# Optimization experiments

Hardware: AMD Instinct MI355X
Metric: run time of the kernel (lower is better)

The kernel has to match this reference:

```python
import jax, jax.numpy as jnp
import numpy as np

B, H, WD, C = 16, 96, 96, 256
WS, SH, NH = 6, 3, 8
N = WS * WS
ALPHA = (2 * 6) ** 0.25  # deepnorm alpha, n_layers=6
SCALE = (C // NH) ** 0.5  # faithful to source: head_dim**0.5 (not **-0.5)
EPS = 1e-5


def _rel_index(ws):
    coords = np.stack(np.meshgrid(np.arange(ws), np.arange(ws), indexing='ij'))  # (2,ws,ws)
    flat = coords.reshape(2, -1)
    rel = (flat[:, :, None] - flat[:, None, :]).transpose(1, 2, 0).copy()
    rel[..., 0] += ws - 1
    rel[..., 1] += ws - 1
    rel[..., 0] *= 2 * ws - 1
    return jnp.asarray(rel.sum(-1))  # (N,N) int


def _attn_mask(h, w, ws, sh):
    img = np.zeros((h, w))
    cnt = 0
    for hs in (slice(0, -ws), slice(-ws, -sh), slice(-sh, None)):
        for wsl in (slice(0, -ws), slice(-ws, -sh), slice(-sh, None)):
            img[hs, wsl] = cnt
            cnt += 1
    win = img.reshape(h // ws, ws, w // ws, ws).transpose(0, 2, 1, 3).reshape(-1, ws * ws)
    diff = win[:, None, :] - win[:, :, None]
    return jnp.asarray(np.where(diff != 0, -100.0, 0.0), jnp.float32)  # (nW,N,N)


def _ln(t, w, b):
    mu = jnp.mean(t, -1, keepdims=True)
    var = jnp.var(t, -1, keepdims=True)
    return (t - mu) * jax.lax.rsqrt(var + EPS) * w + b


def setup_inputs() -> dict:
    key = jax.random.key(0)
    ks = jax.random.split(key, 8)
    d = {
        'x': jax.random.normal(ks[0], (B, H * WD, C), jnp.float32),
        'qkv_w': jax.random.normal(ks[1], (C, 3 * C), jnp.float32) * 0.02,
        'qkv_b': jnp.zeros((3 * C,), jnp.float32),
        'bias_table': jax.random.normal(ks[2], ((2 * WS - 1) ** 2, NH), jnp.float32) * 0.02,
        'proj_w': jax.random.normal(ks[3], (C, C), jnp.float32) * 0.02,
        'proj_b': jnp.zeros((C,), jnp.float32),
        'norm1_w': jnp.ones((C,), jnp.float32),
        'norm1_b': jnp.zeros((C,), jnp.float32),
        'norm2_w': jnp.ones((C,), jnp.float32),
        'norm2_b': jnp.zeros((C,), jnp.float32),
        'fc1_w': jax.random.normal(ks[4], (C, 4 * C), jnp.float32) * 0.02,
        'fc1_b': jnp.zeros((4 * C,), jnp.float32),
        'fc2_w': jax.random.normal(ks[5], (4 * C, C), jnp.float32) * 0.02,
        'fc2_b': jnp.zeros((C,), jnp.float32),
    }
    return d


def reference(x, qkv_w, qkv_b, bias_table, proj_w, proj_b, norm1_w, norm1_b,
              norm2_w, norm2_b, fc1_w, fc1_b, fc2_w, fc2_b):
    hd = C // NH
    nW = (H // WS) * (WD // WS)
    shortcut = x  # (B, L, C), norm_before=False -> post-norm
    xs = x.reshape(B, H, WD, C)
    xs = jnp.roll(xs, (-SH, -SH), axis=(1, 2))  # cyclic shift
    # window partition -> (B*nW, N, C)
    xw = xs.reshape(B, H // WS, WS, WD // WS, WS, C).transpose(0, 1, 3, 2, 4, 5).reshape(B * nW, N, C)
    qkv = (xw @ qkv_w + qkv_b).reshape(B * nW, N, 3, NH, hd).transpose(2, 0, 3, 1, 4)
    q, k, v = qkv[0] * SCALE, qkv[1], qkv[2]
    attn = jnp.einsum('bhnd,bhmd->bhnm', q, k)  # (B*nW, H, N, N)
    bias = bias_table[_rel_index(WS).reshape(-1)].reshape(N, N, NH).transpose(2, 0, 1)
    attn = attn + bias[None]
    mask = _attn_mask(H, WD, WS, SH)  # (nW, N, N)
    attn = attn.reshape(B, nW, NH, N, N) + mask[None, :, None]
    attn = jax.nn.softmax(attn.reshape(B * nW, NH, N, N), axis=-1)
    out = jnp.einsum('bhnm,bhmd->bhnd', attn, v).transpose(0, 2, 1, 3).reshape(B * nW, N, C)
    out = out @ proj_w + proj_b
    # faithful buggy window_reverse: identity permute == plain reshape
    xs = out.reshape(B, H // WS, WS, WD // WS, WS, C).reshape(B, H, WD, C)
    xs = jnp.roll(xs, (SH, SH), axis=(1, 2))
    x1 = _ln(shortcut * ALPHA + xs.reshape(B, H * WD, C), norm1_w, norm1_b)
    hmid = jax.nn.gelu(x1 @ fc1_w + fc1_b, approximate=False)
    x2 = _ln(x1 * ALPHA + (hmid @ fc2_w + fc2_b), norm2_w, norm2_b)
    return x2
```

## Files before the change

kernel.cpp:

```cpp
#include <hip/hip_runtime.h>
#include <math.h>

typedef __bf16 bf16x8 __attribute__((ext_vector_type(8)));
typedef __bf16 bf16x4 __attribute__((ext_vector_type(4)));
typedef short  s16x4  __attribute__((ext_vector_type(4)));
typedef float  f32x4  __attribute__((ext_vector_type(4)));

#define NTOK 147456
#define LTOK 9216
#define ALPHA 1.8612097182041991f
#define QSCALE 5.656854249492380196f
#define MFMA32(a,b,c) __builtin_amdgcn_mfma_f32_16x16x32_bf16((a),(b),(c),0,0,0)
#define SWB(row,kb) ((kb) ^ ((row)&7))

__device__ __forceinline__ f32x4 MFMA16(bf16x4 a, bf16x4 b, f32x4 c) {
#if __has_builtin(__builtin_amdgcn_mfma_f32_16x16x16bf16_1k)
    return __builtin_amdgcn_mfma_f32_16x16x16bf16_1k(*(s16x4*)&a, *(s16x4*)&b, c, 0, 0, 0);
#else
    f32x4 d = c;
    asm volatile("s_nop 1\n\ts_nop 1\n\t"
                 "v_mfma_f32_16x16x16_bf16 %0, %1, %2, %0\n\t"
                 "s_nop 7\n\ts_nop 7"
                 : "+v"(d) : "v"(a), "v"(b));
    return d;
#endif
}

__device__ __forceinline__ float gelu_sig(float x) {
    const float e = __expf(-1.702f * x);
    return x * __builtin_amdgcn_rcpf(1.0f + e);
}

__device__ __forceinline__ void gll16(const void* g, void* l) {
    __builtin_amdgcn_global_load_lds(
        (const __attribute__((address_space(1))) void*)g,
        (__attribute__((address_space(3))) void*)l, 16, 0, 0);
}

__global__ __launch_bounds__(256) void k0_prep(
    const float* __restrict__ qkv_w, const float* __restrict__ proj_w,
    const float* __restrict__ fc1_w, const float* __restrict__ fc2_w,
    __bf16* __restrict__ qkvT, __bf16* __restrict__ projT,
    __bf16* __restrict__ w1T, __bf16* __restrict__ w2T)
{
    const int id = blockIdx.x * 256 + threadIdx.x;
    if (id < 196608) {
        const int o = id >> 8, k = id & 255;
        qkvT[id] = (__bf16)qkv_w[k * 768 + o];
    } else if (id < 262144) {
        const int i = id - 196608, o = i >> 8, k = i & 255;
        projT[i] = (__bf16)proj_w[k * 256 + o];
    } else if (id < 524288) {
        const int i = id - 262144, o = i >> 8, k = i & 255;
        w1T[i] = (__bf16)fc1_w[k * 1024 + o];
    } else {
        const int i = id - 524288, o = i >> 10, k = i & 1023;
        w2T[i] = (__bf16)fc2_w[k * 256 + o];
    }
}

__global__ __launch_bounds__(512, 4) void k1f_qkv_attn(
    const float* __restrict__ x, const __bf16* __restrict__ qkvT,
    const float* __restrict__ qkv_b, const float* __restrict__ bias_table,
    __bf16* __restrict__ attnout)
{
    __shared__ __attribute__((aligned(16))) char SM[77824];
    typedef __bf16 (*a256_t)[256];
    typedef __bf16 (*b32_t)[32];
    a256_t As = (a256_t)SM;
    b32_t  Bs = (b32_t)(SM + 24576);
    int*   srcrow = (int*)(SM + 73728);
    float* bias_s = (float*)(SM + 73920);

    const int t = threadIdx.x;
    const int wid = t >> 6, lane = t & 63;
    const int l15 = lane & 15, lg = lane >> 4;
    const int blk = blockIdx.x;
    const int win = blk & 255;
    const int wh = win >> 4, ww = win & 15;
    const int h = wid;

    if (t < 48) {
        int n = t; if (n > 35) n = 35;
        const int b = blk >> 8;
        const int gh = (wh * 6 + n / 6 + 3) % 96;
        const int gw = (ww * 6 + n % 6 + 3) % 96;
        srcrow[t] = b * LTOK + gh * 96 + gw;
    }
    for (int o = t; o < 968; o += 512) bias_s[o] = bias_table[o];
    __syncthreads();

    for (int o = t; o < 48 * 32; o += 512) {
        const int row = o >> 5, kb = o & 31;
        const float* src = x + (size_t)srcrow[row] * 256 + kb * 8;
        const float4 f0 = *(const float4*)src;
        const float4 f1 = *(const float4*)(src + 4);
        bf16x8 p;
        p[0] = (__bf16)f0.x; p[1] = (__bf16)f0.y; p[2] = (__bf16)f0.z; p[3] = (__bf16)f0.w;
        p[4] = (__bf16)f1.x; p[5] = (__bf16)f1.y; p[6] = (__bf16)f1.z; p[7] = (__bf16)f1.w;
        *(bf16x8*)&As[row][SWB(row, kb) * 8] = p;
    }

    const f32x4 fzero = {0.f, 0.f, 0.f, 0.f};
    f32x4 accQ[2][3], accK[2][3], accV[2][3];
    #pragma unroll
    for (int c = 0; c < 2; ++c)
        #pragma unroll
        for (int r = 0; r < 3; ++r) { accQ[c][r] = fzero; accK[c][r] = fzero; accV[c][r] = fzero; }

    for (int kc = 0; kc < 8; ++kc) {
        __syncthreads();
        #pragma unroll
        for (int i = 0; i < 6; ++i) {
            const int r0 = wid * 96 + i * 16;
            const int row = r0 + (lane >> 2), kbl = lane & 3;
            gll16(qkvT + (size_t)row * 256 + kc * 32 + ((kbl ^ (row & 3)) * 8),
                  &Bs[r0][0]);
        }
        __syncthreads();
        bf16x8 af[3];
        #pragma unroll
        for (int rt = 0; rt < 3; ++rt) {
            const int ar = rt * 16 + l15;
            const int kb = kc * 4 + lg;
            af[rt] = *(const bf16x8*)&As[ar][SWB(ar, kb) * 8];
        }
        #pragma unroll
        for (int ct = 0; ct < 2; ++ct) {
            const int brq = h * 32 + ct * 16 + l15;
            const bf16x8 bq = *(const bf16x8*)&Bs[brq][((lg ^ (brq & 3))) * 8];
            const int brk = 256 + brq;
            const bf16x8 bk = *(const bf16x8*)&Bs[brk][((lg ^ (brk & 3))) * 8];
            const int brv = 512 + brq;
            const bf16x8 bv = *(const bf16x8*)&Bs[brv][((lg ^ (brv & 3))) * 8];
            #pragma unroll
            for (int rt = 0; rt < 3; ++rt) {
                accQ[ct][rt] = MFMA32(bq, af[rt], accQ[ct][rt]);
                accK[ct][rt] = MFMA32(bk, af[rt], accK[ct][rt]);
                accV[ct][rt] = MFMA32(af[rt], bv, accV[ct][rt]);
            }
        }
    }

    bf16x4 qf[3][2], kf[3][2], vf[2][3];
    #pragma unroll
    for (int dh = 0; dh < 2; ++dh) {
        #pragma unroll
        for (int q = 0; q < 4; ++q) {
            const float qb = qkv_b[h * 32 + dh * 16 + lg * 4 + q];
            const float kb = qkv_b[256 + h * 32 + dh * 16 + lg * 4 + q];
            #pragma unroll
            for (int rt = 0; rt < 3; ++rt) {
                qf[rt][dh][q] = (__bf16)((accQ[dh][rt][q] + qb) * QSCALE);
                kf[rt][dh][q] = (__bf16)(accK[dh][rt][q] + kb);
            }
        }
    }
    #pragma unroll
    for (int cd = 0; cd < 2; ++cd) {
        const float vb = qkv_b[512 + h * 32 + cd * 16 + l15];
        #pragma unroll
        for (int c3 = 0; c3 < 3; ++c3)
            #pragma unroll
            for (int q = 0; q < 4; ++q)
                vf[cd][c3][q] = (__bf16)(accV[cd][c3][q] + vb);
    }

    f32x4 s[3][3];
    #pragma unroll
    for (int qt = 0; qt < 3; ++qt)
        #pragma unroll
        for (int c3 = 0; c3 < 3; ++c3) {
            f32x4 acc = MFMA16(kf[c3][0], qf[qt][0], fzero);
            s[qt][c3] = MFMA16(kf[c3][1], qf[qt][1], acc);
        }

    int i2_[3][4], j2_[3][4], g2_[3][4];
    #pragma unroll
    for (int c3 = 0; c3 < 3; ++c3)
        #pragma unroll
        for (int q = 0; q < 4; ++q) {
            const int kt = c3 * 16 + lg * 4 + q;
            const int kk2 = kt < 36 ? kt : 35;
            i2_[c3][q] = kk2 / 6; j2_[c3][q] = kk2 - i2_[c3][q] * 6;
            g2_[c3][q] = ((wh < 15) ? 0 : (i2_[c3][q] < 3 ? 1 : 2)) * 3
                       + ((ww < 15) ? 0 : (j2_[c3][q] < 3 ? 1 : 2));
        }

    bf16x4 pa[3][3];
    #pragma unroll
    for (int qt = 0; qt < 3; ++qt) {
        const int qtok = qt * 16 + l15;
        const int nn = qtok < 36 ? qtok : 35;
        const int i1 = nn / 6, j1 = nn - i1 * 6;
        const int g1 = ((wh < 15) ? 0 : (i1 < 3 ? 1 : 2)) * 3
                     + ((ww < 15) ? 0 : (j1 < 3 ? 1 : 2));
        float vals[3][4];
        float mx = -1e30f;
        #pragma unroll
        for (int c3 = 0; c3 < 3; ++c3)
            #pragma unroll
            for (int q = 0; q < 4; ++q) {
                const int kt = c3 * 16 + lg * 4 + q;
                float v;
                if (kt < 36) {
                    v = s[qt][c3][q]
                      + bias_s[((i1 - i2_[c3][q] + 5) * 11 + (j1 - j2_[c3][q] + 5)) * 8 + h];
                    if (g1 != g2_[c3][q]) v -= 100.0f;
                } else {
                    v = -1e30f;
                }
                vals[c3][q] = v;
                mx = fmaxf(mx, v);
            }
        mx = fmaxf(mx, __shfl_xor(mx, 16));
        mx = fmaxf(mx, __shfl_xor(mx, 32));
        float sum = 0.f;
        #pragma unroll
        for (int c3 = 0; c3 < 3; ++c3)
            #pragma unroll
            for (int q = 0; q < 4; ++q) {
                const float e = __expf(vals[c3][q] - mx);
                vals[c3][q] = e;
                sum += e;
            }
        sum += __shfl_xor(sum, 16);
        sum += __shfl_xor(sum, 32);
        const float inv = 1.0f / sum;
        #pragma unroll
        for (int c3 = 0; c3 < 3; ++c3)
            #pragma unroll
            for (int q = 0; q < 4; ++q)
                pa[qt][c3][q] = (__bf16)(vals[c3][q] * inv);
    }

    const size_t rowbase = (size_t)blk * 36;
    #pragma unroll
    for (int qt = 0; qt < 3; ++qt)
        #pragma unroll
        for (int cd = 0; cd < 2; ++cd) {
            f32x4 o = MFMA16(pa[qt][0], vf[cd][0], fzero);
            o = MFMA16(pa[qt][1], vf[cd][1], o);
            o = MFMA16(pa[qt][2], vf[cd][2], o);
            #pragma unroll
            for (int q = 0; q < 4; ++q) {
                const int n = qt * 16 + lg * 4 + q;
                if (n < 36)
                    attnout[(rowbase + n) * 256 + h * 32 + cd * 16 + l15] = (__bf16)o[q];
            }
        }
}

__global__ __launch_bounds__(512) void k2_proj_ln(
    const __bf16* __restrict__ attnout, const __bf16* __restrict__ projT,
    const float* __restrict__ proj_b, const float* __restrict__ x,
    const float* __restrict__ n1w, const float* __restrict__ n1b,
    __bf16* __restrict__ x1b)
{
    __shared__ __attribute__((aligned(16))) __bf16 As[128][64];
    __shared__ __attribute__((aligned(16))) __bf16 Bs[256][64];
    __shared__ float ps[128][4], ps2[128][4];
    const int t = threadIdx.x;
    const int wid = t >> 6, lane = t & 63;
    const int l15 = lane & 15, lg = lane >> 4;
    const int mb = blockIdx.x;
    const int wm = wid >> 2, wn = wid & 3;

    const f32x4 fzero = {0.f, 0.f, 0.f, 0.f};
    f32x4 acc[4][4];
    #pragma unroll
    for (int i = 0; i < 4; ++i)
        #pragma unroll
        for (int j = 0; j < 4; ++j) acc[i][j] = fzero;

    for (int kc = 0; kc < 4; ++kc) {
        __syncthreads();
        #pragma unroll
        for (int i = 0; i < 2; ++i) {
            const int r0 = wid * 16 + i * 8;
            const int row = r0 + (lane >> 3), kbl = lane & 7;
            gll16(attnout + (size_t)(mb * 128 + row) * 256 + kc * 64 + ((kbl ^ (row & 7)) * 8),
                  &As[r0][0]);
        }
        #pragma unroll
        for (int i = 0; i < 4; ++i) {
            const int r0 = wid * 32 + i * 8;
            const int row = r0 + (lane >> 3), kbl = lane & 7;
            gll16(projT + (size_t)row * 256 + kc * 64 + ((kbl ^ (row & 7)) * 8),
                  &Bs[r0][0]);
        }
        __syncthreads();
        #pragma unroll
        for (int kk = 0; kk < 2; ++kk) {
            bf16x8 af[4], bfr[4];
            #pragma unroll
            for (int rt = 0; rt < 4; ++rt) {
                const int ar = wm * 64 + rt * 16 + l15;
                af[rt] = *(const bf16x8*)&As[ar][((kk * 4 + lg) ^ (ar & 7)) * 8];
            }
            #pragma unroll
            for (int ct = 0; ct < 4; ++ct) {
                const int br = wn * 64 + ct * 16 + l15;
                bfr[ct] = *(const bf16x8*)&Bs[br][((kk * 4 + lg) ^ (br & 7)) * 8];
            }
            #pragma unroll
            for (int rt = 0; rt < 4; ++rt)
                #pragma unroll
                for (int ct = 0; ct < 4; ++ct)
                    acc[rt][ct] = MFMA32(af[rt], bfr[ct], acc[rt][ct]);
        }
    }

    int dtok_[4][4];
    #pragma unroll
    for (int rt = 0; rt < 4; ++rt) {
        #pragma unroll
        for (int q = 0; q < 4; ++q) {
            const int rowl = wm * 64 + rt * 16 + lg * 4 + q;
            const int tok = mb * 128 + rowl;
            const int b = tok / LTOK, l = tok % LTOK;
            const int hh = l / 96, wwp = l % 96;
            const int dtok = b * LTOK + ((hh + 3) % 96) * 96 + ((wwp + 3) % 96);
            dtok_[rt][q] = dtok;
            float s = 0.f, s2 = 0.f;
            #pragma unroll
            for (int ct = 0; ct < 4; ++ct) {
                const int col = wn * 64 + ct * 16 + l15;
                const float v = acc[rt][ct][q] + proj_b[col] + ALPHA * x[(size_t)dtok * 256 + col];
                acc[rt][ct][q] = v;
                s += v; s2 += v * v;
            }
            s  += __shfl_xor(s, 1, 16);  s += __shfl_xor(s, 2, 16);
            s  += __shfl_xor(s, 4, 16);  s += __shfl_xor(s, 8, 16);
            s2 += __shfl_xor(s2, 1, 16); s2 += __shfl_xor(s2, 2, 16);
            s2 += __shfl_xor(s2, 4, 16); s2 += __shfl_xor(s2, 8, 16);
            if (l15 == 0) { ps[rowl][wn] = s; ps2[rowl][wn] = s2; }
        }
    }
    __syncthreads();
    #pragma unroll
    for (int rt = 0; rt < 4; ++rt) {
        #pragma unroll
        for (int q = 0; q < 4; ++q) {
            const int rowl = wm * 64 + rt * 16 + lg * 4 + q;
            const float S  = ps[rowl][0] + ps[rowl][1] + ps[rowl][2] + ps[rowl][3];
            const float S2 = ps2[rowl][0] + ps2[rowl][1] + ps2[rowl][2] + ps2[rowl][3];
            const float mu = S * (1.0f / 256.0f);
            const float var = S2 * (1.0f / 256.0f) - mu * mu;
            const float rstd = rsqrtf(var + 1e-5f);
            __bf16* op = x1b + (size_t)dtok_[rt][q] * 256;
            #pragma unroll
            for (int ct = 0; ct < 4; ++ct) {
                const int col = wn * 64 + ct * 16 + l15;
                op[col] = (__bf16)((acc[rt][ct][q] - mu) * rstd * n1w[col] + n1b[col]);
            }
        }
    }
}

__global__ __launch_bounds__(512, 2) void k3f_mlp(
    const __bf16* __restrict__ x1b, const __bf16* __restrict__ w1T,
    const float* __restrict__ fc1_b, const __bf16* __restrict__ w2T,
    const float* __restrict__ fc2_b, const float* __restrict__ n2w,
    const float* __restrict__ n2b, float* __restrict__ out)
{
    __shared__ __attribute__((aligned(16))) __bf16 w1c[2][64][256];
    __shared__ __attribute__((aligned(16))) __bf16 w2c[2][256][64];
    __shared__ float ps[128][2], ps2[128][2];

    const int t = threadIdx.x;
    const int wid = t >> 6, lane = t & 63;
    const int l15 = lane & 15, lg = lane >> 4;
    const int rg = wid >> 1, chs = wid & 1;
    const int rowbase = blockIdx.x * 128 + rg * 32;

    bf16x8 af[2][8];
    #pragma unroll
    for (int tt = 0; tt < 2; ++tt)
        #pragma unroll
        for (int kk = 0; kk < 8; ++kk)
            af[tt][kk] = *(const bf16x8*)(x1b + (size_t)(rowbase + tt * 16 + l15) * 256 + kk * 32 + lg * 8);

    const f32x4 fzero = {0.f, 0.f, 0.f, 0.f};
    f32x4 acc2[2][8];
    #pragma unroll
    for (int i = 0; i < 2; ++i)
        #pragma unroll
        for (int j = 0; j < 8; ++j) acc2[i][j] = fzero;

    #define STAGE_W(b, c)                                                       \
    {                                                                           \
        _Pragma("unroll")                                                       \
        for (int i = 0; i < 4; ++i) {                                           \
            const int r0 = wid * 8 + i * 2;                                     \
            const int row = r0 + (lane >> 5);                                   \
            const int g = (lane & 31) ^ (row & 7);                              \
            gll16(w1T + (size_t)((c) * 64 + row) * 256 + g * 8, &w1c[b][r0][0]);\
        }                                                                       \
        _Pragma("unroll")                                                       \
        for (int i = 0; i < 4; ++i) {                                           \
            const int r0 = wid * 32 + i * 8;                                    \
            const int row = r0 + (lane >> 3);                                   \
            const int g = (lane & 7) ^ (row & 7);                               \
            gll16(w2T + (size_t)row * 1024 + (c) * 64 + g * 8, &w2c[b][r0][0]); \
        }                                                                       \
    }

    STAGE_W(0, 0);
    __syncthreads();

    for (int ch = 0; ch < 16; ++ch) {
        const int cur = ch & 1;
        if (ch < 15) STAGE_W(cur ^ 1, ch + 1);

        f32x4 acc1[4][2];
        #pragma unroll
        for (int i = 0; i < 4; ++i)
            #pragma unroll
            for (int j = 0; j < 2; ++j) acc1[i][j] = fzero;
        #pragma unroll
        for (int kk = 0; kk < 8; ++kk) {
            #pragma unroll
            for (int ht = 0; ht < 4; ++ht) {
                const int hr = ht * 16 + l15;
                const bf16x8 aW = *(const bf16x8*)&w1c[cur][hr][((kk * 4 + lg) ^ (hr & 7)) * 8];
                #pragma unroll
                for (int tt = 0; tt < 2; ++tt)
                    acc1[ht][tt] = MFMA32(aW, af[tt][kk], acc1[ht][tt]);
            }
        }

        bf16x4 a16[2][4];
        #pragma unroll
        for (int ht = 0; ht < 4; ++ht) {
            float bq[4];
            #pragma unroll
            for (int q = 0; q < 4; ++q)
                bq[q] = fc1_b[ch * 64 + ht * 16 + lg * 4 + q];
            #pragma unroll
            for (int tt = 0; tt < 2; ++tt)
                #pragma unroll
                for (int q = 0; q < 4; ++q)
                    a16[tt][ht][q] = (__bf16)gelu_sig(acc1[ht][tt][q] + bq[q]);
        }

        #pragma unroll
        for (int ht = 0; ht < 4; ++ht) {
            #pragma unroll
            for (int ct = 0; ct < 8; ++ct) {
                const int br = chs * 128 + ct * 16 + l15;
                const bf16x4 bW = *(const bf16x4*)&w2c[cur][br]
                    [((ht * 2 + (lg >> 1)) ^ (br & 7)) * 8 + (lg & 1) * 4];
                #pragma unroll
                for (int tt = 0; tt < 2; ++tt)
                    acc2[tt][ct] = MFMA16(a16[tt][ht], bW, acc2[tt][ct]);
            }
        }

        __syncthreads();
    }

    #pragma unroll
    for (int tt = 0; tt < 2; ++tt) {
        #pragma unroll
        for (int q = 0; q < 4; ++q) {
            const int grow = rg * 32 + tt * 16 + lg * 4 + q;
            const size_t tok = (size_t)(blockIdx.x * 128 + grow);
            float s = 0.f, s2 = 0.f;
            #pragma unroll
            for (int ct = 0; ct < 8; ++ct) {
                const int col = chs * 128 + ct * 16 + l15;
                const float v = acc2[tt][ct][q] + fc2_b[col] + ALPHA * (float)x1b[tok * 256 + col];
                acc2[tt][ct][q] = v;
                s += v; s2 += v * v;
            }
            s  += __shfl_xor(s, 1, 16);  s += __shfl_xor(s, 2, 16);
            s  += __shfl_xor(s, 4, 16);  s += __shfl_xor(s, 8, 16);
            s2 += __shfl_xor(s2, 1, 16); s2 += __shfl_xor(s2, 2, 16);
            s2 += __shfl_xor(s2, 4, 16); s2 += __shfl_xor(s2, 8, 16);
            if (l15 == 0) { ps[grow][chs] = s; ps2[grow][chs] = s2; }
        }
    }
    __syncthreads();
    #pragma unroll
    for (int tt = 0; tt < 2; ++tt) {
        #pragma unroll
        for (int q = 0; q < 4; ++q) {
            const int grow = rg * 32 + tt * 16 + lg * 4 + q;
            const size_t tok = (size_t)(blockIdx.x * 128 + grow);
            const float S  = ps[grow][0] + ps[grow][1];
            const float S2 = ps2[grow][0] + ps2[grow][1];
            const float mu = S * (1.0f / 256.0f);
            const float var = S2 * (1.0f / 256.0f) - mu * mu;
            const float rstd = rsqrtf(var + 1e-5f);
            float* op = out + tok * 256;
            #pragma unroll
            for (int ct = 0; ct < 8; ++ct) {
                const int col = chs * 128 + ct * 16 + l15;
                op[col] = (acc2[tt][ct][q] - mu) * rstd * n2w[col] + n2b[col];
            }
        }
    }
    #undef STAGE_W
}

extern "C" void kernel_launch(void* const* d_in, const int* in_sizes, int n_in,
                              void* d_out, int out_size, void* d_ws, size_t ws_size,
                              hipStream_t stream)
{
    const float* x          = (const float*)d_in[0];
    const float* qkv_w      = (const float*)d_in[1];
    const float* qkv_b      = (const float*)d_in[2];
    const float* bias_table = (const float*)d_in[3];
    const float* proj_w     = (const float*)d_in[4];
    const float* proj_b     = (const float*)d_in[5];
    const float* n1w        = (const float*)d_in[6];
    const float* n1b        = (const float*)d_in[7];
    const float* n2w        = (const float*)d_in[8];
    const float* n2b        = (const float*)d_in[9];
    const float* fc1_w      = (const float*)d_in[10];
    const float* fc1_b      = (const float*)d_in[11];
    const float* fc2_w      = (const float*)d_in[12];
    const float* fc2_b      = (const float*)d_in[13];
    float* out = (float*)d_out;

    char* ws = (char*)d_ws;
    __bf16* x1b     = (__bf16*)ws;
    __bf16* attnout = (__bf16*)(ws + 75497472);
    __bf16* qkvT    = (__bf16*)(ws + 150994944);
    __bf16* projT   = (__bf16*)(ws + 151388160);
    __bf16* w1T     = (__bf16*)(ws + 151519232);
    __bf16* w2T     = (__bf16*)(ws + 152043520);

    k0_prep<<<3072, 256, 0, stream>>>(qkv_w, proj_w, fc1_w, fc2_w, qkvT, projT, w1T, w2T);
    k1f_qkv_attn<<<4096, 512, 0, stream>>>(x, qkvT, qkv_b, bias_table, attnout);
    k2_proj_ln<<<1152, 512, 0, stream>>>(attnout, projT, proj_b, x, n1w, n1b, x1b);
    k3f_mlp<<<1152, 512, 0, stream>>>(x1b, w1T, fc1_b, w2T, fc2_b, n2w, n2b, out);
}
```

Before: 733.8 us.

## Restructure MLP kernel to 4 waves with full-width rows and LDS-staged hidden

```diff
diff --git a/kernel.cpp b/kernel.cpp
--- a/kernel.cpp
+++ b/kernel.cpp
@@ -358,21 +358,20 @@
     }
 }
 
-__global__ __launch_bounds__(512, 2) void k3f_mlp(
+__global__ __launch_bounds__(256, 2) void k3f_mlp(
     const __bf16* __restrict__ x1b, const __bf16* __restrict__ w1T,
     const float* __restrict__ fc1_b, const __bf16* __restrict__ w2T,
     const float* __restrict__ fc2_b, const float* __restrict__ n2w,
     const float* __restrict__ n2b, float* __restrict__ out)
 {
-    __shared__ __attribute__((aligned(16))) __bf16 w1c[2][64][256];
-    __shared__ __attribute__((aligned(16))) __bf16 w2c[2][256][64];
-    __shared__ float ps[128][2], ps2[128][2];
+    __shared__ __attribute__((aligned(16))) __bf16 w1c[2][32][256];
+    __shared__ __attribute__((aligned(16))) __bf16 w2c[2][256][32];
+    __shared__ __attribute__((aligned(16))) __bf16 hs[4][32][32];
 
     const int t = threadIdx.x;
-    const int wid = t >> 6, lane = t & 63;
+    const int wv = t >> 6, lane = t & 63;
     const int l15 = lane & 15, lg = lane >> 4;
-    const int rg = wid >> 1, chs = wid & 1;
-    const int rowbase = blockIdx.x * 128 + rg * 32;
+    const int rowbase = blockIdx.x * 128 + wv * 32;
 
     bf16x8 af[2][8];
     #pragma unroll
@@ -382,46 +381,49 @@
             af[tt][kk] = *(const bf16x8*)(x1b + (size_t)(rowbase + tt * 16 + l15) * 256 + kk * 32 + lg * 8);
 
     const f32x4 fzero = {0.f, 0.f, 0.f, 0.f};
-    f32x4 acc2[2][8];
+    f32x4 acc2[2][16];
     #pragma unroll
     for (int i = 0; i < 2; ++i)
         #pragma unroll
-        for (int j = 0; j < 8; ++j) acc2[i][j] = fzero;
-
-    #define STAGE_W(b, c)                                                       \
-    {                                                                           \
-        _Pragma("unroll")                                                       \
-        for (int i = 0; i < 4; ++i) {                                           \
-            const int r0 = wid * 8 + i * 2;                                     \
-            const int row = r0 + (lane >> 5);                                   \
-            const int g = (lane & 31) ^ (row & 7);                              \
-            gll16(w1T + (size_t)((c) * 64 + row) * 256 + g * 8, &w1c[b][r0][0]);\
-        }                                                                       \
-        _Pragma("unroll")                                                       \
-        for (int i = 0; i < 4; ++i) {                                           \
-            const int r0 = wid * 32 + i * 8;                                    \
-            const int row = r0 + (lane >> 3);                                   \
-            const int g = (lane & 7) ^ (row & 7);                               \
-            gll16(w2T + (size_t)row * 1024 + (c) * 64 + g * 8, &w2c[b][r0][0]); \
-        }                                                                       \
+        for (int j = 0; j < 16; ++j) acc2[i][j] = fzero;
+
+    #define STAGE_W(b, c)                                                        \
+    {                                                                            \
+        _Pragma("unroll")                                                        \
+        for (int i = 0; i < 4; ++i) {                                            \
+            const int r0 = wv * 8 + i * 2;                                       \
+            const int row = r0 + (lane >> 5);                                    \
+            const int g = (lane & 31) ^ (row & 7);                               \
+            gll16(w1T + (size_t)((c) * 32 + row) * 256 + g * 8, &w1c[b][r0][0]); \
+        }                                                                        \
+        _Pragma("unroll")                                                        \
+        for (int i = 0; i < 4; ++i) {                                            \
+            const int r0 = wv * 64 + i * 16;                                     \
+            const int row = r0 + (lane >> 2);                                    \
+            const int g = (lane & 3) ^ (row & 3);                                \
+            gll16(w2T + (size_t)row * 1024 + (c) * 32 + g * 8, &w2c[b][r0][0]);  \
+        }                                                                        \
     }
 
     STAGE_W(0, 0);
-    __syncthreads();
-
-    for (int ch = 0; ch < 16; ++ch) {
+    asm volatile("s_waitcnt vmcnt(0)" ::: "memory");
+    __builtin_amdgcn_sched_barrier(0);
+    __builtin_amdgcn_s_barrier();
+    __builtin_amdgcn_sched_barrier(0);
+
+    for (int ch = 0; ch < 32; ++ch) {
         const int cur = ch & 1;
-        if (ch < 15) STAGE_W(cur ^ 1, ch + 1);
-
-        f32x4 acc1[4][2];
-        #pragma unroll
-        for (int i = 0; i < 4; ++i)
+        if (ch < 31) STAGE_W(cur ^ 1, ch + 1);
+
+        f32x4 acc1[2][2];
+        #pragma unroll
+        for (int i = 0; i < 2; ++i)
             #pragma unroll
             for (int j = 0; j < 2; ++j) acc1[i][j] = fzero;
         #pragma unroll
         for (int kk = 0; kk < 8; ++kk) {
             #pragma unroll
-            for (int ht = 0; ht < 4; ++ht) {
+            for (int ht = 0; ht < 2; ++ht) {
                 const int hr = ht * 16 + l15;
                 const bf16x8 aW = *(const bf16x8*)&w1c[cur][hr][((kk * 4 + lg) ^ (hr & 7)) * 8];
                 #pragma unroll
@@ -430,74 +432,72 @@
             }
         }
 
-        bf16x4 a16[2][4];
-        #pragma unroll
-        for (int ht = 0; ht < 4; ++ht) {
+        #pragma unroll
+        for (int ht = 0; ht < 2; ++ht) {
             float bq[4];
             #pragma unroll
             for (int q = 0; q < 4; ++q)
-                bq[q] = fc1_b[ch * 64 + ht * 16 + lg * 4 + q];
-            #pragma unroll
-            for (int tt = 0; tt < 2; ++tt)
+                bq[q] = fc1_b[ch * 32 + ht * 16 + lg * 4 + q];
+            #pragma unroll
+            for (int tt = 0; tt < 2; ++tt) {
+                bf16x4 p;
                 #pragma unroll
                 for (int q = 0; q < 4; ++q)
-                    a16[tt][ht][q] = (__bf16)gelu_sig(acc1[ht][tt][q] + bq[q]);
-        }
-
-        #pragma unroll
-        for (int ht = 0; ht < 4; ++ht) {
-            #pragma unroll
-            for (int ct = 0; ct < 8; ++ct) {
-                const int br = chs * 128 + ct * 16 + l15;
-                const bf16x4 bW = *(const bf16x4*)&w2c[cur][br]
-                    [((ht * 2 + (lg >> 1)) ^ (br & 7)) * 8 + (lg & 1) * 4];
-                #pragma unroll
-                for (int tt = 0; tt < 2; ++tt)
-                    acc2[tt][ct] = MFMA16(a16[tt][ht], bW, acc2[tt][ct]);
-            }
-        }
-
-        __syncthreads();
+                    p[q] = (__bf16)gelu_sig(acc1[ht][tt][q] + bq[q]);
+                const int row = tt * 16 + l15;
+                const int gW = ht * 2 + (lg >> 1);
+                *(bf16x4*)&hs[wv][row][(gW ^ (row & 3)) * 8 + (lg & 1) * 4] = p;
+            }
+        }
+
+        bf16x8 a2[2];
+        #pragma unroll
+        for (int tt = 0; tt < 2; ++tt) {
+            const int row = tt * 16 + l15;
+            a2[tt] = *(const bf16x8*)&hs[wv][row][((lg ^ (row & 3))) * 8];
+        }
+        #pragma unroll
+        for (int ct = 0; ct < 16; ++ct) {
+            const int br = ct * 16 + l15;
+            const bf16x8 bW = *(const bf16x8*)&w2c[cur][br][((lg ^ (br & 3))) * 8];
+            #pragma unroll
+            for (int tt = 0; tt < 2; ++tt)
+                acc2[tt][ct] = MFMA32(a2[tt], bW, acc2[tt][ct]);
+        }
+
+        asm volatile("s_waitcnt vmcnt(0)" ::: "memory");
+        __builtin_amdgcn_sched_barrier(0);
+        __builtin_amdgcn_s_barrier();
+        __builtin_amdgcn_sched_barrier(0);
     }
 
     #pragma unroll
     for (int tt = 0; tt < 2; ++tt) {
         #pragma unroll
         for (int q = 0; q < 4; ++q) {
-            const int grow = rg * 32 + tt * 16 + lg * 4 + q;
-            const size_t tok = (size_t)(blockIdx.x * 128 + grow);
+            const int grow = tt * 16 + lg * 4 + q;
+            const size_t tok = (size_t)(rowbase + grow);
             float s = 0.f, s2 = 0.f;
-            #pragma unroll
-            for (int ct = 0; ct < 8; ++ct) {
-                const int col = chs * 128 + ct * 16 + l15;
+            float vals[16];
+            #pragma unroll
+            for (int ct = 0; ct < 16; ++ct) {
+                const int col = ct * 16 + l15;
                 const float v = acc2[tt][ct][q] + fc2_b[col] + ALPHA * (float)x1b[tok * 256 + col];
-                acc2[tt][ct][q] = v;
+                vals[ct] = v;
                 s += v; s2 += v * v;
             }
             s  += __shfl_xor(s, 1, 16);  s += __shfl_xor(s, 2, 16);
             s  += __shfl_xor(s, 4, 16);  s += __shfl_xor(s, 8, 16);
             s2 += __shfl_xor(s2, 1, 16); s2 += __shfl_xor(s2, 2, 16);
             s2 += __shfl_xor(s2, 4, 16); s2 += __shfl_xor(s2, 8, 16);
-            if (l15 == 0) { ps[grow][chs] = s; ps2[grow][chs] = s2; }
-        }
-    }
-    __syncthreads();
-    #pragma unroll
-    for (int tt = 0; tt < 2; ++tt) {
-        #pragma unroll
-        for (int q = 0; q < 4; ++q) {
-            const int grow = rg * 32 + tt * 16 + lg * 4 + q;
-            const size_t tok = (size_t)(blockIdx.x * 128 + grow);
-            const float S  = ps[grow][0] + ps[grow][1];
-            const float S2 = ps2[grow][0] + ps2[grow][1];
-            const float mu = S * (1.0f / 256.0f);
-            const float var = S2 * (1.0f / 256.0f) - mu * mu;
+            const float mu = s * (1.0f / 256.0f);
+            const float var = s2 * (1.0f / 256.0f) - mu * mu;
             const float rstd = rsqrtf(var + 1e-5f);
             float* op = out + tok * 256;
             #pragma unroll
-            for (int ct = 0; ct < 8; ++ct) {
-                const int col = chs * 128 + ct * 16 + l15;
-                op[col] = (acc2[tt][ct][q] - mu) * rstd * n2w[col] + n2b[col];
+            for (int ct = 0; ct < 16; ++ct) {
+                const int col = ct * 16 + l15;
+                op[col] = (vals[ct] - mu) * rstd * n2w[col] + n2b[col];
             }
         }
     }
@@ -535,5 +535,5 @@
     k0_prep<<<3072, 256, 0, stream>>>(qkv_w, proj_w, fc1_w, fc2_w, qkvT, projT, w1T, w2T);
     k1f_qkv_attn<<<4096, 512, 0, stream>>>(x, qkvT, qkv_b, bias_table, attnout);
     k2_proj_ln<<<1152, 512, 0, stream>>>(attnout, projT, proj_b, x, n1w, n1b, x1b);
-    k3f_mlp<<<1152, 512, 0, stream>>>(x1b, w1T, fc1_b, w2T, fc2_b, n2w, n2b, out);
-}
+    k3f_mlp<<<1152, 256, 0, stream>>>(x1b, w1T, fc1_b, w2T, fc2_b, n2w, n2b, out);
+}
```

Measured after the change: 626.8 us. -14.6%, faster.
